# Kernel tuning notes

Measured on AMD Instinct MI355X. Metric: run time of the kernel, lower is better.

The kernel has to match this reference:

```python
import jax, jax.numpy as jnp
import numpy as np

N = 100000   # nodes
E = 1600000  # edges
S = 2000     # subgraphs
G = 64       # graphs
H = 64       # hidden
L = 3        # extra GIN layers after conv1 (num_layers=4)
OUT = 8      # OUTPUT_DIM


def setup_inputs() -> dict:
    key = jax.random.key(0)
    ks = jax.random.split(key, 20)
    s = 0.1
    return {
        "x": jax.random.normal(ks[0], (N, 1), jnp.float32),
        "edge_index": jax.random.randint(ks[1], (2, E), 0, N),
        "node_to_subgraph": jnp.sort(jax.random.randint(ks[2], (N,), 0, S)),
        "subgraph_to_graph": jnp.sort(jax.random.randint(ks[3], (S,), 0, G)),
        # conv1 MLP: Linear(1,H) -> ReLU -> Linear(H,H) -> ReLU
        "conv1_w1": jax.random.normal(ks[4], (1, H), jnp.float32) * s,
        "conv1_b1": jnp.zeros((H,), jnp.float32),
        "conv1_w2": jax.random.normal(ks[5], (H, H), jnp.float32) * s,
        "conv1_b2": jnp.zeros((H,), jnp.float32),
        # remaining L GIN layers, stacked: Linear(H,H) -> ReLU -> Linear(H,H) -> ReLU
        "convs_w1": jax.random.normal(ks[6], (L, H, H), jnp.float32) * s,
        "convs_b1": jnp.zeros((L, H), jnp.float32),
        "convs_w2": jax.random.normal(ks[7], (L, H, H), jnp.float32) * s,
        "convs_b2": jnp.zeros((L, H), jnp.float32),
        "lin1_w": jax.random.normal(ks[8], (H, H), jnp.float32) * s,
        "lin1_b": jnp.zeros((H,), jnp.float32),
        "lin2_w": jax.random.normal(ks[9], (H, OUT), jnp.float32) * s,
        "lin2_b": jnp.zeros((OUT,), jnp.float32),
    }


def _gin_layer(x, src, dst, w1, b1, w2, b2):
    # GINConv with eps=0: mlp(x + sum_{j in N(i)} x_j)
    agg = jax.ops.segment_sum(x[src], dst, num_segments=N)
    h = x + agg
    h = jax.nn.relu(h @ w1 + b1)
    return jax.nn.relu(h @ w2 + b2)


def reference(x, edge_index, node_to_subgraph, subgraph_to_graph,
              conv1_w1, conv1_b1, conv1_w2, conv1_b2,
              convs_w1, convs_b1, convs_w2, convs_b2,
              lin1_w, lin1_b, lin2_w, lin2_b):
    src, dst = edge_index[0], edge_index[1]
    h = _gin_layer(x, src, dst, conv1_w1, conv1_b1, conv1_w2, conv1_b2)
    for i in range(L):
        h = _gin_layer(h, src, dst, convs_w1[i], convs_b1[i], convs_w2[i], convs_b2[i])
    # node -> subgraph -> graph double add-pool
    h = jax.ops.segment_sum(h, node_to_subgraph, num_segments=S)
    h = jax.ops.segment_sum(h, subgraph_to_graph, num_segments=G)
    h = jax.nn.relu(h @ lin1_w + lin1_b)
    h = h @ lin2_w + lin2_b
    return jax.nn.log_softmax(h, axis=-1)
```

## Files before the change

kernel.cpp:

```cpp
#include <hip/hip_runtime.h>
#include <hip/hip_bf16.h>

#define N_NODES 100000
#define N_EDGES 1600000
#define N_SUB   2000
#define N_GRAPH 64
#define HID     64
#define NLAYERS 3
#define SCAN_B  1024
#define N_SCANB ((N_NODES + SCAN_B - 1) / SCAN_B)

__device__ __forceinline__ float bcastf(float v, int l) {
  return __int_as_float(__builtin_amdgcn_readlane(__float_as_int(v), l));
}

__global__ __launch_bounds__(256) void count_slot_kernel(
    const int4* __restrict__ dst4, int* __restrict__ deg,
    int4* __restrict__ slot4) {
  int t = blockIdx.x * blockDim.x + threadIdx.x;
  int nt = gridDim.x * blockDim.x;
  for (int e4 = t; e4 < N_EDGES / 4; e4 += nt) {
    int4 d = dst4[e4];
    int4 p;
    p.x = atomicAdd(&deg[d.x], 1);
    p.y = atomicAdd(&deg[d.y], 1);
    p.z = atomicAdd(&deg[d.z], 1);
    p.w = atomicAdd(&deg[d.w], 1);
    slot4[e4] = p;
  }
}

__global__ __launch_bounds__(SCAN_B) void scan_block_kernel(
    const int* __restrict__ deg, int* __restrict__ rowptr,
    int* __restrict__ partials) {
  __shared__ int sm[SCAN_B];
  const int tid = threadIdx.x;
  const int g = blockIdx.x * SCAN_B + tid;
  int v = (g < N_NODES) ? deg[g] : 0;
  sm[tid] = v;
  __syncthreads();
  for (int off = 1; off < SCAN_B; off <<= 1) {
    int t = (tid >= off) ? sm[tid - off] : 0;
    __syncthreads();
    sm[tid] += t;
    __syncthreads();
  }
  if (g < N_NODES) rowptr[g] = sm[tid] - v;
  if (tid == SCAN_B - 1) partials[blockIdx.x] = sm[tid];
}

__global__ __launch_bounds__(128) void scan_partials_kernel(int* partials) {
  __shared__ int sm[128];
  const int tid = threadIdx.x;
  int v = (tid < N_SCANB) ? partials[tid] : 0;
  sm[tid] = v;
  __syncthreads();
  for (int off = 1; off < 128; off <<= 1) {
    int t = (tid >= off) ? sm[tid - off] : 0;
    __syncthreads();
    sm[tid] += t;
    __syncthreads();
  }
  if (tid < N_SCANB) partials[tid] = sm[tid] - v;
}

__global__ __launch_bounds__(SCAN_B) void add_offsets_kernel(
    int* __restrict__ rowptr, const int* __restrict__ partials) {
  const int g = blockIdx.x * SCAN_B + threadIdx.x;
  if (g < N_NODES) rowptr[g] += partials[blockIdx.x];
  if (g == 0) rowptr[N_NODES] = N_EDGES;
}

__global__ __launch_bounds__(256) void fill_csr2_kernel(
    const int4* __restrict__ src4, const int4* __restrict__ dst4,
    const int4* __restrict__ slot4, const int* __restrict__ rowptr,
    int* __restrict__ csr) {
  int t = blockIdx.x * blockDim.x + threadIdx.x;
  int nt = gridDim.x * blockDim.x;
  for (int e4 = t; e4 < N_EDGES / 4; e4 += nt) {
    int4 s = src4[e4];
    int4 d = dst4[e4];
    int4 p = slot4[e4];
    csr[rowptr[d.x] + p.x] = s.x;
    csr[rowptr[d.y] + p.y] = s.y;
    csr[rowptr[d.z] + p.z] = s.z;
    csr[rowptr[d.w] + p.w] = s.w;
  }
}

__global__ __launch_bounds__(256) void conv1_agg_kernel(
    const float* __restrict__ x, const int* __restrict__ rowptr,
    const int* __restrict__ csr, float* __restrict__ agg1) {
  int t = blockIdx.x * blockDim.x + threadIdx.x;
  int nt = gridDim.x * blockDim.x;
  for (int i = t; i < N_NODES; i += nt) {
    float a = x[i];
    int end = rowptr[i + 1];
    for (int e = rowptr[i]; e < end; e++) a += x[csr[e]];
    agg1[i] = a;
  }
}

__global__ __launch_bounds__(256) void conv1_mlp(
    const float* __restrict__ agg1,
    const float* __restrict__ w1, const float* __restrict__ b1,
    const float* __restrict__ w2, const float* __restrict__ b2,
    float* __restrict__ h) {
  const int lane = threadIdx.x & 63;
  const int wid = (blockIdx.x * blockDim.x + threadIdx.x) >> 6;
  const int nw = (gridDim.x * blockDim.x) >> 6;
  const float w1l = w1[lane], b1l = b1[lane], b2l = b2[lane];
  float w2c[64];
#pragma unroll
  for (int k = 0; k < 64; k++) w2c[k] = w2[k * 64 + lane];

  for (int i = wid; i < N_NODES; i += nw) {
    float hv = agg1[i];
    float y1 = fmaxf(hv * w1l + b1l, 0.f);
    float a0 = b2l, a1 = 0.f, a2 = 0.f, a3 = 0.f;
#pragma unroll
    for (int k = 0; k < 64; k += 4) {
      a0 += bcastf(y1, k)     * w2c[k];
      a1 += bcastf(y1, k + 1) * w2c[k + 1];
      a2 += bcastf(y1, k + 2) * w2c[k + 2];
      a3 += bcastf(y1, k + 3) * w2c[k + 3];
    }
    h[i * 64 + lane] = fmaxf(a0 + a1 + a2 + a3, 0.f);
  }
}

__global__ __launch_bounds__(256) void gather64_f4_kernel(
    const float4* __restrict__ h4, const int* __restrict__ rowptr,
    const int* __restrict__ csr, float4* __restrict__ agg4) {
  const int lane = threadIdx.x & 63;
  const int q = lane >> 4;
  const int sub = lane & 15;
  const int wid = (blockIdx.x * blockDim.x + threadIdx.x) >> 6;
  const int nw = (gridDim.x * blockDim.x) >> 6;
  for (int i = wid; i < N_NODES; i += nw) {
    const int beg = rowptr[i], end = rowptr[i + 1];
    float ax = 0.f, ay = 0.f, az = 0.f, aw = 0.f;
    for (int c = beg; c < end; c += 64) {
      const int nb = min(64, end - c);
      int idx = csr[c + min(lane, nb - 1)];
      int j = 0;
      for (; j + 16 <= nb; j += 16) {
        int s0 = __shfl(idx, j + q, 64);
        int s1 = __shfl(idx, j + 4 + q, 64);
        int s2 = __shfl(idx, j + 8 + q, 64);
        int s3 = __shfl(idx, j + 12 + q, 64);
        float4 v0 = h4[(size_t)s0 * 16 + sub];
        float4 v1 = h4[(size_t)s1 * 16 + sub];
        float4 v2 = h4[(size_t)s2 * 16 + sub];
        float4 v3 = h4[(size_t)s3 * 16 + sub];
        ax += (v0.x + v1.x) + (v2.x + v3.x);
        ay += (v0.y + v1.y) + (v2.y + v3.y);
        az += (v0.z + v1.z) + (v2.z + v3.z);
        aw += (v0.w + v1.w) + (v2.w + v3.w);
      }
      for (; j < nb; j += 4) {
        int li = j + q;
        int s = __shfl(idx, li < nb ? li : 0, 64);
        float4 v = h4[(size_t)s * 16 + sub];
        if (li < nb) { ax += v.x; ay += v.y; az += v.z; aw += v.w; }
      }
    }
    ax += __shfl_xor(ax, 16, 64); ay += __shfl_xor(ay, 16, 64);
    az += __shfl_xor(az, 16, 64); aw += __shfl_xor(aw, 16, 64);
    ax += __shfl_xor(ax, 32, 64); ay += __shfl_xor(ay, 32, 64);
    az += __shfl_xor(az, 32, 64); aw += __shfl_xor(aw, 32, 64);
    if (q == 0) {
      float4 self = h4[(size_t)i * 16 + sub];
      float4 r;
      r.x = ax + self.x; r.y = ay + self.y;
      r.z = az + self.z; r.w = aw + self.w;
      agg4[(size_t)i * 16 + sub] = r;
    }
  }
}

__global__ __launch_bounds__(256) void gin_mlp3(
    const float* __restrict__ agg,
    const float* __restrict__ w1, const float* __restrict__ b1,
    const float* __restrict__ w2, const float* __restrict__ b2,
    float* __restrict__ h) {
  const int lane = threadIdx.x & 63;
  const int wid = (blockIdx.x * blockDim.x + threadIdx.x) >> 6;
  const int nw = (gridDim.x * blockDim.x) >> 6;
  const float b1l = b1[lane], b2l = b2[lane];
  float w1c[64], w2c[64];
#pragma unroll
  for (int k = 0; k < 64; k++) {
    w1c[k] = w1[k * 64 + lane];
    w2c[k] = w2[k * 64 + lane];
  }

  for (int i0 = wid; i0 < N_NODES; i0 += nw) {
    const int i = __builtin_amdgcn_readfirstlane(i0);
    const float* __restrict__ arow = agg + (size_t)i * 64;
    float a0 = b1l, a1 = 0.f, a2 = 0.f, a3 = 0.f;
#pragma unroll
    for (int k = 0; k < 64; k += 4) {
      a0 = fmaf(arow[k],     w1c[k],     a0);
      a1 = fmaf(arow[k + 1], w1c[k + 1], a1);
      a2 = fmaf(arow[k + 2], w1c[k + 2], a2);
      a3 = fmaf(arow[k + 3], w1c[k + 3], a3);
    }
    float y1 = fmaxf(a0 + a1 + a2 + a3, 0.f);
    a0 = b2l; a1 = 0.f; a2 = 0.f; a3 = 0.f;
#pragma unroll
    for (int k = 0; k < 64; k += 4) {
      a0 = fmaf(bcastf(y1, k),     w2c[k],     a0);
      a1 = fmaf(bcastf(y1, k + 1), w2c[k + 1], a1);
      a2 = fmaf(bcastf(y1, k + 2), w2c[k + 2], a2);
      a3 = fmaf(bcastf(y1, k + 3), w2c[k + 3], a3);
    }
    h[(size_t)i * 64 + lane] = fmaxf(a0 + a1 + a2 + a3, 0.f);
  }
}

__global__ __launch_bounds__(256) void pool_nodes(
    const float* __restrict__ h, const int* __restrict__ n2s,
    float* __restrict__ sub) {
  const int lane = threadIdx.x & 63;
  const int wid = (blockIdx.x * blockDim.x + threadIdx.x) >> 6;
  const int nw = (gridDim.x * blockDim.x) >> 6;
  for (int i = wid; i < N_NODES; i += nw) {
    int s = n2s[i];
    atomicAdd(&sub[s * 64 + lane], h[i * 64 + lane]);
  }
}

__global__ __launch_bounds__(256) void pool_sub(
    const float* __restrict__ sub, const int* __restrict__ s2g,
    float* __restrict__ gp) {
  const int lane = threadIdx.x & 63;
  const int wid = (blockIdx.x * blockDim.x + threadIdx.x) >> 6;
  const int nw = (gridDim.x * blockDim.x) >> 6;
  for (int s = wid; s < N_SUB; s += nw) {
    int g = s2g[s];
    atomicAdd(&gp[g * 64 + lane], sub[s * 64 + lane]);
  }
}

__global__ __launch_bounds__(64) void head_kernel(
    const float* __restrict__ gp,
    const float* __restrict__ w1, const float* __restrict__ b1,
    const float* __restrict__ w2, const float* __restrict__ b2,
    float* __restrict__ out) {
  const int g = blockIdx.x;
  const int lane = threadIdx.x;
  float v = gp[g * 64 + lane];
  float acc = b1[lane];
#pragma unroll
  for (int k = 0; k < 64; k++) acc += bcastf(v, k) * w1[k * 64 + lane];
  float y1 = fmaxf(acc, 0.f);
  const int o = lane & 7;
  float acc2 = b2[o];
#pragma unroll
  for (int k = 0; k < 64; k++) acc2 += bcastf(y1, k) * w2[k * 8 + o];
  float m = -1e30f;
#pragma unroll
  for (int oo = 0; oo < 8; oo++) m = fmaxf(m, bcastf(acc2, oo));
  float s = 0.f;
#pragma unroll
  for (int oo = 0; oo < 8; oo++) s += expf(bcastf(acc2, oo) - m);
  float ls = logf(s);
  if (lane < 8) out[g * 8 + lane] = acc2 - m - ls;
}

extern "C" void kernel_launch(void* const* d_in, const int* in_sizes, int n_in,
                              void* d_out, int out_size, void* d_ws,
                              size_t ws_size, hipStream_t stream) {
  const float* x   = (const float*)d_in[0];
  const int* ei    = (const int*)d_in[1];
  const int* src   = ei;
  const int* dst   = ei + N_EDGES;
  const int* n2s   = (const int*)d_in[2];
  const int* s2g   = (const int*)d_in[3];
  const float* c1w1 = (const float*)d_in[4];
  const float* c1b1 = (const float*)d_in[5];
  const float* c1w2 = (const float*)d_in[6];
  const float* c1b2 = (const float*)d_in[7];
  const float* cw1  = (const float*)d_in[8];
  const float* cb1  = (const float*)d_in[9];
  const float* cw2  = (const float*)d_in[10];
  const float* cb2  = (const float*)d_in[11];
  const float* l1w  = (const float*)d_in[12];
  const float* l1b  = (const float*)d_in[13];
  const float* l2w  = (const float*)d_in[14];
  const float* l2b  = (const float*)d_in[15];

  char* p = (char*)d_ws;
  float* h      = (float*)p;  p += (size_t)N_NODES * 64 * 4;
  float* agg    = (float*)p;  p += (size_t)N_NODES * 64 * 4;
  int*   csr    = (int*)p;    p += (size_t)N_EDGES * 4;
  int*   rowptr = (int*)p;    p += (size_t)(N_NODES + 1) * 4;
  int*   deg    = (int*)p;    p += (size_t)N_NODES * 4;
  int*   part   = (int*)p;    p += 256 * 4;
  float* agg1   = (float*)p;  p += (size_t)N_NODES * 4;
  float* sub    = (float*)p;  p += (size_t)N_SUB * 64 * 4;
  float* gp     = (float*)p;  p += (size_t)N_GRAPH * 64 * 4;
  if ((size_t)(p - (char*)d_ws) > ws_size) return;

  int* slot = (int*)agg;

  float* outf = (float*)d_out;

  hipMemsetAsync(deg, 0, N_NODES * sizeof(int), stream);
  count_slot_kernel<<<2048, 256, 0, stream>>>(
      (const int4*)dst, deg, (int4*)slot);
  scan_block_kernel<<<N_SCANB, SCAN_B, 0, stream>>>(deg, rowptr, part);
  scan_partials_kernel<<<1, 128, 0, stream>>>(part);
  add_offsets_kernel<<<N_SCANB, SCAN_B, 0, stream>>>(rowptr, part);
  fill_csr2_kernel<<<2048, 256, 0, stream>>>(
      (const int4*)src, (const int4*)dst, (const int4*)slot, rowptr, csr);

  conv1_agg_kernel<<<1024, 256, 0, stream>>>(x, rowptr, csr, agg1);
  conv1_mlp<<<2048, 256, 0, stream>>>(agg1, c1w1, c1b1, c1w2, c1b2, h);

  for (int l = 0; l < NLAYERS; l++) {
    gather64_f4_kernel<<<2048, 256, 0, stream>>>(
        (const float4*)h, rowptr, csr, (float4*)agg);
    gin_mlp3<<<2048, 256, 0, stream>>>(
        agg, cw1 + l * 64 * 64, cb1 + l * 64, cw2 + l * 64 * 64,
        cb2 + l * 64, h);
  }

  hipMemsetAsync(sub, 0, N_SUB * 64 * sizeof(float), stream);
  hipMemsetAsync(gp, 0, N_GRAPH * 64 * sizeof(float), stream);
  pool_nodes<<<1024, 256, 0, stream>>>(h, n2s, sub);
  pool_sub<<<64, 256, 0, stream>>>(sub, s2g, gp);
  head_kernel<<<N_GRAPH, 64, 0, stream>>>(gp, l1w, l1b, l2w, l2b, outf);
}
```

Baseline: 586.9 us.

## Fuse neighbor gather with GIN MLP and fold node pooling into last layer

Merges the per-layer gather kernel and the MLP kernel into one kernel that keeps the aggregated row in registers and runs both linear layers with lane broadcasts. This removes the write and re-read of the N x 64 aggregate buffer each layer. The final layer atomically adds into the subgraph sums directly, so the separate pool_nodes pass is dropped. Two ping-pong node buffers replace the in-place update. Holding 128 weight registers per lane alongside the gather state may lower occupancy and limit latency hiding for the random gathers.

```diff
diff --git a/kernel.cpp b/kernel.cpp
--- a/kernel.cpp
+++ b/kernel.cpp
@@ -129,14 +129,27 @@
   }
 }
 
-__global__ __launch_bounds__(256) void gather64_f4_kernel(
+template <bool POOL>
+__global__ __launch_bounds__(256) void gin_layer_fused(
     const float4* __restrict__ h4, const int* __restrict__ rowptr,
-    const int* __restrict__ csr, float4* __restrict__ agg4) {
+    const int* __restrict__ csr,
+    const float* __restrict__ w1, const float* __restrict__ b1,
+    const float* __restrict__ w2, const float* __restrict__ b2,
+    const int* __restrict__ n2s,
+    float* __restrict__ hout, float* __restrict__ subp) {
   const int lane = threadIdx.x & 63;
   const int q = lane >> 4;
-  const int sub = lane & 15;
+  const int su = lane & 15;
   const int wid = (blockIdx.x * blockDim.x + threadIdx.x) >> 6;
   const int nw = (gridDim.x * blockDim.x) >> 6;
+  const float b1l = b1[lane], b2l = b2[lane];
+  float w1c[64], w2c[64];
+#pragma unroll
+  for (int k = 0; k < 64; k++) {
+    w1c[k] = w1[k * 64 + lane];
+    w2c[k] = w2[k * 64 + lane];
+  }
+
   for (int i = wid; i < N_NODES; i += nw) {
     const int beg = rowptr[i], end = rowptr[i + 1];
     float ax = 0.f, ay = 0.f, az = 0.f, aw = 0.f;
@@ -149,10 +162,10 @@
         int s1 = __shfl(idx, j + 4 + q, 64);
         int s2 = __shfl(idx, j + 8 + q, 64);
         int s3 = __shfl(idx, j + 12 + q, 64);
-        float4 v0 = h4[(size_t)s0 * 16 + sub];
-        float4 v1 = h4[(size_t)s1 * 16 + sub];
-        float4 v2 = h4[(size_t)s2 * 16 + sub];
-        float4 v3 = h4[(size_t)s3 * 16 + sub];
+        float4 v0 = h4[(size_t)s0 * 16 + su];
+        float4 v1 = h4[(size_t)s1 * 16 + su];
+        float4 v2 = h4[(size_t)s2 * 16 + su];
+        float4 v3 = h4[(size_t)s3 * 16 + su];
         ax += (v0.x + v1.x) + (v2.x + v3.x);
         ay += (v0.y + v1.y) + (v2.y + v3.y);
         az += (v0.z + v1.z) + (v2.z + v3.z);
@@ -161,7 +174,7 @@
       for (; j < nb; j += 4) {
         int li = j + q;
         int s = __shfl(idx, li < nb ? li : 0, 64);
-        float4 v = h4[(size_t)s * 16 + sub];
+        float4 v = h4[(size_t)s * 16 + su];
         if (li < nb) { ax += v.x; ay += v.y; az += v.z; aw += v.w; }
       }
     }
@@ -169,65 +182,35 @@
     az += __shfl_xor(az, 16, 64); aw += __shfl_xor(aw, 16, 64);
     ax += __shfl_xor(ax, 32, 64); ay += __shfl_xor(ay, 32, 64);
     az += __shfl_xor(az, 32, 64); aw += __shfl_xor(aw, 32, 64);
-    if (q == 0) {
-      float4 self = h4[(size_t)i * 16 + sub];
-      float4 r;
-      r.x = ax + self.x; r.y = ay + self.y;
-      r.z = az + self.z; r.w = aw + self.w;
-      agg4[(size_t)i * 16 + sub] = r;
-    }
-  }
-}
-
-__global__ __launch_bounds__(256) void gin_mlp3(
-    const float* __restrict__ agg,
-    const float* __restrict__ w1, const float* __restrict__ b1,
-    const float* __restrict__ w2, const float* __restrict__ b2,
-    float* __restrict__ h) {
-  const int lane = threadIdx.x & 63;
-  const int wid = (blockIdx.x * blockDim.x + threadIdx.x) >> 6;
-  const int nw = (gridDim.x * blockDim.x) >> 6;
-  const float b1l = b1[lane], b2l = b2[lane];
-  float w1c[64], w2c[64];
-#pragma unroll
-  for (int k = 0; k < 64; k++) {
-    w1c[k] = w1[k * 64 + lane];
-    w2c[k] = w2[k * 64 + lane];
-  }
-
-  for (int i0 = wid; i0 < N_NODES; i0 += nw) {
-    const int i = __builtin_amdgcn_readfirstlane(i0);
-    const float* __restrict__ arow = agg + (size_t)i * 64;
-    float a0 = b1l, a1 = 0.f, a2 = 0.f, a3 = 0.f;
+    float4 self = h4[(size_t)i * 16 + su];
+    const float a0 = ax + self.x, a1 = ay + self.y;
+    const float a2 = az + self.z, a3 = aw + self.w;
+
+    float c0 = b1l, c1 = 0.f, c2 = 0.f, c3 = 0.f;
+#pragma unroll
+    for (int j = 0; j < 16; j++) {
+      c0 = fmaf(bcastf(a0, j), w1c[4 * j],     c0);
+      c1 = fmaf(bcastf(a1, j), w1c[4 * j + 1], c1);
+      c2 = fmaf(bcastf(a2, j), w1c[4 * j + 2], c2);
+      c3 = fmaf(bcastf(a3, j), w1c[4 * j + 3], c3);
+    }
+    float y1 = fmaxf(c0 + c1 + c2 + c3, 0.f);
+
+    c0 = b2l; c1 = 0.f; c2 = 0.f; c3 = 0.f;
 #pragma unroll
     for (int k = 0; k < 64; k += 4) {
-      a0 = fmaf(arow[k],     w1c[k],     a0);
-      a1 = fmaf(arow[k + 1], w1c[k + 1], a1);
-      a2 = fmaf(arow[k + 2], w1c[k + 2], a2);
-      a3 = fmaf(arow[k + 3], w1c[k + 3], a3);
-    }
-    float y1 = fmaxf(a0 + a1 + a2 + a3, 0.f);
-    a0 = b2l; a1 = 0.f; a2 = 0.f; a3 = 0.f;
-#pragma unroll
-    for (int k = 0; k < 64; k += 4) {
-      a0 = fmaf(bcastf(y1, k),     w2c[k],     a0);
-      a1 = fmaf(bcastf(y1, k + 1), w2c[k + 1], a1);
-      a2 = fmaf(bcastf(y1, k + 2), w2c[k + 2], a2);
-      a3 = fmaf(bcastf(y1, k + 3), w2c[k + 3], a3);
-    }
-    h[(size_t)i * 64 + lane] = fmaxf(a0 + a1 + a2 + a3, 0.f);
-  }
-}
-
-__global__ __launch_bounds__(256) void pool_nodes(
-    const float* __restrict__ h, const int* __restrict__ n2s,
-    float* __restrict__ sub) {
-  const int lane = threadIdx.x & 63;
-  const int wid = (blockIdx.x * blockDim.x + threadIdx.x) >> 6;
-  const int nw = (gridDim.x * blockDim.x) >> 6;
-  for (int i = wid; i < N_NODES; i += nw) {
-    int s = n2s[i];
-    atomicAdd(&sub[s * 64 + lane], h[i * 64 + lane]);
+      c0 = fmaf(bcastf(y1, k),     w2c[k],     c0);
+      c1 = fmaf(bcastf(y1, k + 1), w2c[k + 1], c1);
+      c2 = fmaf(bcastf(y1, k + 2), w2c[k + 2], c2);
+      c3 = fmaf(bcastf(y1, k + 3), w2c[k + 3], c3);
+    }
+    float y2 = fmaxf(c0 + c1 + c2 + c3, 0.f);
+
+    if (POOL) {
+      atomicAdd(&subp[(size_t)n2s[i] * 64 + lane], y2);
+    } else {
+      hout[(size_t)i * 64 + lane] = y2;
+    }
   }
 }
 
@@ -293,7 +276,7 @@
 
   char* p = (char*)d_ws;
   float* h      = (float*)p;  p += (size_t)N_NODES * 64 * 4;
-  float* agg    = (float*)p;  p += (size_t)N_NODES * 64 * 4;
+  float* h2     = (float*)p;  p += (size_t)N_NODES * 64 * 4;
   int*   csr    = (int*)p;    p += (size_t)N_EDGES * 4;
   int*   rowptr = (int*)p;    p += (size_t)(N_NODES + 1) * 4;
   int*   deg    = (int*)p;    p += (size_t)N_NODES * 4;
@@ -303,7 +286,7 @@
   float* gp     = (float*)p;  p += (size_t)N_GRAPH * 64 * 4;
   if ((size_t)(p - (char*)d_ws) > ws_size) return;
 
-  int* slot = (int*)agg;
+  int* slot = (int*)h2;
 
   float* outf = (float*)d_out;
 
@@ -319,17 +302,19 @@
   conv1_agg_kernel<<<1024, 256, 0, stream>>>(x, rowptr, csr, agg1);
   conv1_mlp<<<2048, 256, 0, stream>>>(agg1, c1w1, c1b1, c1w2, c1b2, h);
 
-  for (int l = 0; l < NLAYERS; l++) {
-    gather64_f4_kernel<<<2048, 256, 0, stream>>>(
-        (const float4*)h, rowptr, csr, (float4*)agg);
-    gin_mlp3<<<2048, 256, 0, stream>>>(
-        agg, cw1 + l * 64 * 64, cb1 + l * 64, cw2 + l * 64 * 64,
-        cb2 + l * 64, h);
-  }
-
   hipMemsetAsync(sub, 0, N_SUB * 64 * sizeof(float), stream);
   hipMemsetAsync(gp, 0, N_GRAPH * 64 * sizeof(float), stream);
-  pool_nodes<<<1024, 256, 0, stream>>>(h, n2s, sub);
+
+  gin_layer_fused<false><<<2048, 256, 0, stream>>>(
+      (const float4*)h, rowptr, csr, cw1 + 0 * 4096, cb1 + 0 * 64,
+      cw2 + 0 * 4096, cb2 + 0 * 64, n2s, h2, nullptr);
+  gin_layer_fused<false><<<2048, 256, 0, stream>>>(
+      (const float4*)h2, rowptr, csr, cw1 + 1 * 4096, cb1 + 1 * 64,
+      cw2 + 1 * 4096, cb2 + 1 * 64, n2s, h, nullptr);
+  gin_layer_fused<true><<<2048, 256, 0, stream>>>(
+      (const float4*)h, rowptr, csr, cw1 + 2 * 4096, cb1 + 2 * 64,
+      cw2 + 2 * 4096, cb2 + 2 * 64, n2s, nullptr, sub);
+
   pool_sub<<<64, 256, 0, stream>>>(sub, s2g, gp);
   head_kernel<<<N_GRAPH, 64, 0, stream>>>(gp, l1w, l1b, l2w, l2b, outf);
 }
```

New measurement: 695.7 us. 1.19x slower.
